# Optimization experiments

Hardware: AMD Instinct MI355X
Metric: run time of the kernel (lower is better)

The kernel has to match this reference:

```python
import jax, jax.numpy as jnp
import numpy as np

B, SQ, SKV, D = 4, 4096, 4096, 64

def setup_inputs() -> dict:
    key = jax.random.key(0)
    kq, kv = jax.random.split(key)
    query = jax.random.normal(kq, (B, SQ, D), dtype=jnp.float32)
    value = jax.random.normal(kv, (B, SKV, D), dtype=jnp.float32)
    return {"query": query, "value": value}

def reference(query, value):
    # scores = Q @ V^T  (value acts as both keys and values; no 1/sqrt(d) scaling)
    scores = jnp.einsum('bqd,bkd->bqk', query, value)  # [B, SQ, SKV]
    dist = jax.nn.softmax(scores, axis=-1)
    context = jnp.einsum('bqk,bkd->bqd', dist, value)  # [B, SQ, D]
    return context
```

## Files before the change

### kernel.cpp

```cpp
#include <hip/hip_runtime.h>


#define NB   4
#define SQ   4096
#define SKV  4096
#define DH   64
#define L2E  1.44269504088896340736f

typedef _Float16 half8 __attribute__((ext_vector_type(8)));
typedef _Float16 half4 __attribute__((ext_vector_type(4)));
typedef _Float16 half2v __attribute__((ext_vector_type(2)));
typedef float f32x4 __attribute__((ext_vector_type(4)));
typedef unsigned short u16;

#define MFMA16(a, b, c) __builtin_amdgcn_mfma_f32_16x16x16f16((a), (b), (c), 0, 0, 0)
#define MFMA32(a, b, c) __builtin_amdgcn_mfma_f32_16x16x32_f16((a), (b), (c), 0, 0, 0)

__device__ __forceinline__ u16 f2h(float f) {
  _Float16 h = (_Float16)f;
  return __builtin_bit_cast(u16, h);
}
__device__ __forceinline__ half2v pkrtz(float a, float b) {
  return __builtin_bit_cast(half2v, __builtin_amdgcn_cvt_pkrtz(a, b));
}

__global__ __launch_bounds__(256) void prep_kernel(
    const float* __restrict__ V, u16* __restrict__ vh, u16* __restrict__ vt) {
  __shared__ u16 ldsT[16 * 72];
  int blk = blockIdx.x;
  int b   = blk >> 8;
  int rem = blk & 255;
  int j0  = (rem >> 2) << 6;
  int d0  = (rem & 3) << 4;
  int t   = threadIdx.x;
  int j   = t >> 2;
  int dc  = (t & 3) << 2;

  const float* src = V + ((size_t)(b * SKV) + j0 + j) * DH + d0 + dc;
  float4 v4 = *(const float4*)src;
  u16 h[4] = {f2h(v4.x), f2h(v4.y), f2h(v4.z), f2h(v4.w)};
  unsigned p0 = (unsigned)h[0] | ((unsigned)h[1] << 16);
  unsigned p1 = (unsigned)h[2] | ((unsigned)h[3] << 16);
  size_t go = ((size_t)(b * SKV) + j0 + j) * DH + d0 + dc;
  *(uint2*)(vh + go) = make_uint2(p0, p1);

#pragma unroll
  for (int k = 0; k < 4; ++k) ldsT[(dc + k) * 72 + j] = h[k];
  __syncthreads();

  int dl = t >> 4;
  int jc = (t & 15) << 2;
  u16 tr[4];
#pragma unroll
  for (int k = 0; k < 4; ++k) tr[k] = ldsT[dl * 72 + jc + k];
  unsigned q0 = (unsigned)tr[0] | ((unsigned)tr[1] << 16);
  unsigned q1 = (unsigned)tr[2] | ((unsigned)tr[3] << 16);
  *(uint2*)(vt + ((size_t)(b * DH) + d0 + dl) * SKV + j0 + jc) = make_uint2(q0, q1);
}

__global__ __launch_bounds__(256, 4) void attn_kernel(
    const float* __restrict__ Q,
    const u16* __restrict__ vh,
    const u16* __restrict__ vt,
    u16* __restrict__ po,
    float* __restrict__ pm,
    float* __restrict__ pl,
    int S, int kvLen) {
  __shared__ __align__(16) u16 lds[2][2][64 * 72];

  int blk  = blockIdx.x;
  int tile = blk / S;
  int s    = blk - tile * S;
  int b    = tile >> 5;
  int q0   = (tile & 31) << 7;
  int kv0  = s * kvLen;
  int t    = threadIdx.x;
  int wave = t >> 6;
  int lane = t & 63;
  int col  = lane & 15;
  int quad = lane >> 4;
  int qw   = q0 + (wave << 5);

  half8 qf[2][2];
#pragma unroll
  for (int set = 0; set < 2; ++set) {
#pragma unroll
    for (int kc = 0; kc < 2; ++kc) {
      const float* qp = Q + ((size_t)(b * SQ) + qw + set * 16 + col) * DH +
                        kc * 32 + (quad << 3);
      float4 a0 = *(const float4*)qp;
      float4 a1 = *(const float4*)(qp + 4);
      half8 h;
      h[0] = (_Float16)(a0.x * L2E); h[1] = (_Float16)(a0.y * L2E);
      h[2] = (_Float16)(a0.z * L2E); h[3] = (_Float16)(a0.w * L2E);
      h[4] = (_Float16)(a1.x * L2E); h[5] = (_Float16)(a1.y * L2E);
      h[6] = (_Float16)(a1.z * L2E); h[7] = (_Float16)(a1.w * L2E);
      qf[set][kc] = h;
    }
  }

  f32x4 o[2][4];
  float m_r[2] = {-1e30f, -1e30f};
  float l_r[2] = {0.f, 0.f};
#pragma unroll
  for (int set = 0; set < 2; ++set)
#pragma unroll
    for (int nf = 0; nf < 4; ++nf) o[set][nf] = (f32x4){0.f, 0.f, 0.f, 0.f};

  int sr = t >> 2;
  int sc = (t & 3) << 4;
  const u16* gv  = vh + (size_t)(b * SKV) * DH;
  const u16* gvt = vt + (size_t)(b * DH) * SKV;
  int l0 = sr * 72 + sc;

  {
    size_t g  = (size_t)(kv0 + sr) * DH + sc;
    size_t gt = (size_t)sr * SKV + kv0 + sc;
    *(uint4*)(&lds[0][0][l0])     = *(const uint4*)(gv + g);
    *(uint4*)(&lds[0][0][l0 + 8]) = *(const uint4*)(gv + g + 8);
    *(uint4*)(&lds[0][1][l0])     = *(const uint4*)(gvt + gt);
    *(uint4*)(&lds[0][1][l0 + 8]) = *(const uint4*)(gvt + gt + 8);
  }

  int nIter = kvLen >> 6;
  int cur = 0;
  for (int it = 0; it < nIter; ++it) {
    __syncthreads();

    uint4 a0, a1, c0, c1;
    bool more = (it + 1) < nIter;
    if (more) {
      int j0n = kv0 + ((it + 1) << 6);
      size_t g  = (size_t)(j0n + sr) * DH + sc;
      size_t gt = (size_t)sr * SKV + j0n + sc;
      a0 = *(const uint4*)(gv + g);
      a1 = *(const uint4*)(gv + g + 8);
      c0 = *(const uint4*)(gvt + gt);
      c1 = *(const uint4*)(gvt + gt + 8);
    }

    const u16* sv  = &lds[cur][0][0];
    const u16* svt = &lds[cur][1][0];

    half4 pf[2][4];
#pragma unroll
    for (int set = 0; set < 2; ++set) {
      f32x4 sf[4];
#pragma unroll
      for (int nf = 0; nf < 4; ++nf) sf[nf] = (f32x4){0.f, 0.f, 0.f, 0.f};
#pragma unroll
      for (int nf = 0; nf < 4; ++nf) {
#pragma unroll
        for (int kc = 0; kc < 2; ++kc) {
          half8 av = *(const half8*)(sv + (nf * 16 + col) * 72 + kc * 32 + (quad << 3));
          sf[nf] = MFMA32(av, qf[set][kc], sf[nf]);
        }
      }

      float tm = sf[0][0];
#pragma unroll
      for (int nf = 0; nf < 4; ++nf)
#pragma unroll
        for (int r = 0; r < 4; ++r) tm = fmaxf(tm, sf[nf][r]);
      tm = fmaxf(tm, __shfl_xor(tm, 16, 64));
      tm = fmaxf(tm, __shfl_xor(tm, 32, 64));
      float mn = fmaxf(m_r[set], tm);
      float al = exp2f(m_r[set] - mn);
      m_r[set] = mn;
      float rs = 0.f;
#pragma unroll
      for (int nf = 0; nf < 4; ++nf) {
        float p0 = exp2f(sf[nf][0] - mn);
        float p1 = exp2f(sf[nf][1] - mn);
        float p2 = exp2f(sf[nf][2] - mn);
        float p3 = exp2f(sf[nf][3] - mn);
        rs += (p0 + p1) + (p2 + p3);
        half2v lo = pkrtz(p0, p1);
        half2v hi = pkrtz(p2, p3);
        pf[set][nf] = __builtin_shufflevector(lo, hi, 0, 1, 2, 3);
      }
      l_r[set] = l_r[set] * al + rs;
#pragma unroll
      for (int nf = 0; nf < 4; ++nf)
#pragma unroll
        for (int r = 0; r < 4; ++r) o[set][nf][r] *= al;
    }

#pragma unroll
    for (int kc4 = 0; kc4 < 4; ++kc4) {
#pragma unroll
      for (int nf2 = 0; nf2 < 4; ++nf2) {
        half4 avt = *(const half4*)(svt + (nf2 * 16 + col) * 72 + kc4 * 16 + (quad << 2));
        o[0][nf2] = MFMA16(avt, pf[0][kc4], o[0][nf2]);
        o[1][nf2] = MFMA16(avt, pf[1][kc4], o[1][nf2]);
      }
    }

    if (more) {
      u16* dv  = &lds[cur ^ 1][0][0];
      u16* dvt = &lds[cur ^ 1][1][0];
      *(uint4*)(dv + l0)      = a0;
      *(uint4*)(dv + l0 + 8)  = a1;
      *(uint4*)(dvt + l0)     = c0;
      *(uint4*)(dvt + l0 + 8) = c1;
    }
    cur ^= 1;
  }

#pragma unroll
  for (int set = 0; set < 2; ++set) {
    l_r[set] += __shfl_xor(l_r[set], 16, 64);
    l_r[set] += __shfl_xor(l_r[set], 32, 64);
  }
  int pidx = tile * S + s;
  if (quad == 0) {
#pragma unroll
    for (int set = 0; set < 2; ++set) {
      int row = (wave << 5) + set * 16 + col;
      pm[(size_t)pidx * 128 + row] = m_r[set];
      pl[(size_t)pidx * 128 + row] = l_r[set];
    }
  }

  __syncthreads();
  u16* tp = &lds[0][0][0];
#pragma unroll
  for (int set = 0; set < 2; ++set) {
    int q = (wave << 5) + set * 16 + col;
#pragma unroll
    for (int nf2 = 0; nf2 < 4; ++nf2) {
#pragma unroll
      for (int r2 = 0; r2 < 4; r2 += 2) {
        unsigned pk = (unsigned)f2h(o[set][nf2][r2]) |
                      ((unsigned)f2h(o[set][nf2][r2 + 1]) << 16);
        int d = nf2 * 16 + (quad << 2) + r2;
        *(unsigned*)(tp + q * 72 + d) = pk;
      }
    }
  }
  __syncthreads();
  {
    u16* pob = po + (size_t)pidx * 128 * 64;
    int q = t >> 1, hc = (t & 1) << 5;
    uint4 x0 = *(const uint4*)(tp + q * 72 + hc);
    uint4 x1 = *(const uint4*)(tp + q * 72 + hc + 8);
    uint4 x2 = *(const uint4*)(tp + q * 72 + hc + 16);
    uint4 x3 = *(const uint4*)(tp + q * 72 + hc + 24);
    *(uint4*)(pob + q * 64 + hc)      = x0;
    *(uint4*)(pob + q * 64 + hc + 8)  = x1;
    *(uint4*)(pob + q * 64 + hc + 16) = x2;
    *(uint4*)(pob + q * 64 + hc + 24) = x3;
  }
}

__global__ __launch_bounds__(256) void combine_kernel(
    const u16* __restrict__ po,
    const float* __restrict__ pm,
    const float* __restrict__ pl,
    float* __restrict__ out, int S) {
  int t    = threadIdx.x;
  int rowg = blockIdx.x * 32 + (t >> 3);
  int tile = rowg >> 7;
  int row  = rowg & 127;
  int dc   = (t & 7) << 3;

  float mv[8], lv[8];
  float M = -1e30f;
  for (int s = 0; s < S; ++s) {
    mv[s] = pm[(size_t)(tile * S + s) * 128 + row];
    lv[s] = pl[(size_t)(tile * S + s) * 128 + row];
    M = fmaxf(M, mv[s]);
  }
  float L = 0.f, w[8];
  for (int s = 0; s < S; ++s) {
    w[s] = exp2f(mv[s] - M);
    L += lv[s] * w[s];
  }
  float acc[8] = {0.f, 0.f, 0.f, 0.f, 0.f, 0.f, 0.f, 0.f};
  for (int s = 0; s < S; ++s) {
    const u16* p = po + (size_t)(tile * S + s) * 8192 + row * 64 + dc;
    uint4 raw = *(const uint4*)p;
    half8 x = __builtin_bit_cast(half8, raw);
#pragma unroll
    for (int k = 0; k < 8; ++k) acc[k] += w[s] * (float)x[k];
  }
  float invL = 1.0f / L;
  float* op = out + (size_t)rowg * 64 + dc;
  f32x4 o0 = (f32x4){acc[0], acc[1], acc[2], acc[3]};
  f32x4 o1 = (f32x4){acc[4], acc[5], acc[6], acc[7]};
  *(f32x4*)op       = o0 * invL;
  *(f32x4*)(op + 4) = o1 * invL;
}

extern "C" void kernel_launch(void* const* d_in, const int* in_sizes, int n_in,
                              void* d_out, int out_size, void* d_ws, size_t ws_size,
                              hipStream_t stream) {
  const float* Q = (const float*)d_in[0];
  const float* V = (const float*)d_in[1];
  float* out = (float*)d_out;

  const size_t convBytes = (size_t)2 * NB * SKV * DH * 2;
  auto partBytes = [](int S) {
    return (size_t)NB * 32 * S * ((size_t)128 * 64 * 2 + 128 * 8);
  };
  int S = 8;
  while (S > 1 && ws_size < convBytes + partBytes(S)) S >>= 1;
  int kvLen = SKV / S;

  u16* vh = (u16*)d_ws;
  u16* vt = vh + (size_t)NB * SKV * DH;
  u16* po = vt + (size_t)NB * SKV * DH;
  float* pm = (float*)(po + (size_t)NB * 32 * S * 128 * 64);
  float* pl = pm + (size_t)NB * 32 * S * 128;

  prep_kernel<<<NB * 256, 256, 0, stream>>>(V, vh, vt);
  attn_kernel<<<NB * 32 * S, 256, 0, stream>>>(Q, vh, vt, po, pm, pl, S, kvLen);
  combine_kernel<<<NB * SQ / 32, 256, 0, stream>>>(po, pm, pl, out, S);
}
```

Baseline: 128.3 us.

## Load K/V tiles via global_load_lds DMA with XOR-swizzled layout and smaller query tiles

The prep kernel now writes V and V^T with an XOR-swizzled 8-element chunk order, so the attention kernel can copy tiles straight into unpadded LDS using global_load_lds (bypassing registers) and still read them without bank conflicts. The attention block shrinks from 128 to 64 query rows, one 16-row set per wave, and the KV split factor drops from 8 to 4. Per-wave register use goes down, and the global-to-LDS copies no longer go through VGPRs or need explicit LDS stores. In exchange, each block has less reuse of every loaded KV tile, so the same total KV traffic through LDS is spread over twice as many query tiles. Correctness depends on the DMA lane-to-LDS address mapping matching the swizzle.

```diff
diff --git a/kernel.cpp b/kernel.cpp
--- a/kernel.cpp
+++ b/kernel.cpp
@@ -22,6 +22,12 @@
 }
 __device__ __forceinline__ half2v pkrtz(float a, float b) {
   return __builtin_bit_cast(half2v, __builtin_amdgcn_cvt_pkrtz(a, b));
+}
+
+typedef __attribute__((address_space(1))) void gvoid;
+typedef __attribute__((address_space(3))) void lvoid;
+__device__ __forceinline__ void dma16(const u16* g, u16* l) {
+  __builtin_amdgcn_global_load_lds((gvoid*)g, (lvoid*)l, 16, 0, 0);
 }
 
 __global__ __launch_bounds__(256) void prep_kernel(
@@ -41,8 +47,9 @@
   u16 h[4] = {f2h(v4.x), f2h(v4.y), f2h(v4.z), f2h(v4.w)};
   unsigned p0 = (unsigned)h[0] | ((unsigned)h[1] << 16);
   unsigned p1 = (unsigned)h[2] | ((unsigned)h[3] << 16);
-  size_t go = ((size_t)(b * SKV) + j0 + j) * DH + d0 + dc;
-  *(uint2*)(vh + go) = make_uint2(p0, p1);
+  int dfull = d0 + dc;
+  int physd = ((((dfull >> 3) ^ (j & 7)) << 3)) + (dfull & 7);
+  *(uint2*)(vh + ((size_t)(b * SKV) + j0 + j) * DH + physd) = make_uint2(p0, p1);
 
 #pragma unroll
   for (int k = 0; k < 4; ++k) ldsT[(dc + k) * 72 + j] = h[k];
@@ -55,7 +62,13 @@
   for (int k = 0; k < 4; ++k) tr[k] = ldsT[dl * 72 + jc + k];
   unsigned q0 = (unsigned)tr[0] | ((unsigned)tr[1] << 16);
   unsigned q1 = (unsigned)tr[2] | ((unsigned)tr[3] << 16);
-  *(uint2*)(vt + ((size_t)(b * DH) + d0 + dl) * SKV + j0 + jc) = make_uint2(q0, q1);
+  int d   = d0 + dl;
+  int kc2 = jc >> 5;
+  int g   = (jc >> 4) & 1;
+  int qd  = (jc >> 2) & 3;
+  int hp  = ((kc2 << 2) | qd) ^ (d & 7);
+  *(uint2*)(vt + ((size_t)(b * DH) + d) * SKV + j0 + (hp << 3) + (g << 2)) =
+      make_uint2(q0, q1);
 }
 
 __global__ __launch_bounds__(256, 4) void attn_kernel(
@@ -66,97 +79,86 @@
     float* __restrict__ pm,
     float* __restrict__ pl,
     int S, int kvLen) {
-  __shared__ __align__(16) u16 lds[2][2][64 * 72];
+  __shared__ __align__(16) u16 lds[2][2][4096];
 
   int blk  = blockIdx.x;
   int tile = blk / S;
   int s    = blk - tile * S;
-  int b    = tile >> 5;
-  int q0   = (tile & 31) << 7;
+  int b    = tile >> 6;
+  int q0   = (tile & 63) << 6;
   int kv0  = s * kvLen;
   int t    = threadIdx.x;
   int wave = t >> 6;
   int lane = t & 63;
   int col  = lane & 15;
   int quad = lane >> 4;
-  int qw   = q0 + (wave << 5);
-
-  half8 qf[2][2];
-#pragma unroll
-  for (int set = 0; set < 2; ++set) {
-#pragma unroll
-    for (int kc = 0; kc < 2; ++kc) {
-      const float* qp = Q + ((size_t)(b * SQ) + qw + set * 16 + col) * DH +
-                        kc * 32 + (quad << 3);
-      float4 a0 = *(const float4*)qp;
-      float4 a1 = *(const float4*)(qp + 4);
-      half8 h;
-      h[0] = (_Float16)(a0.x * L2E); h[1] = (_Float16)(a0.y * L2E);
-      h[2] = (_Float16)(a0.z * L2E); h[3] = (_Float16)(a0.w * L2E);
-      h[4] = (_Float16)(a1.x * L2E); h[5] = (_Float16)(a1.y * L2E);
-      h[6] = (_Float16)(a1.z * L2E); h[7] = (_Float16)(a1.w * L2E);
-      qf[set][kc] = h;
-    }
-  }
-
-  f32x4 o[2][4];
-  float m_r[2] = {-1e30f, -1e30f};
-  float l_r[2] = {0.f, 0.f};
-#pragma unroll
-  for (int set = 0; set < 2; ++set)
-#pragma unroll
-    for (int nf = 0; nf < 4; ++nf) o[set][nf] = (f32x4){0.f, 0.f, 0.f, 0.f};
-
-  int sr = t >> 2;
-  int sc = (t & 3) << 4;
+  int qw   = q0 + (wave << 4);
+  int c7   = col & 7;
+
   const u16* gv  = vh + (size_t)(b * SKV) * DH;
   const u16* gvt = vt + (size_t)(b * DH) * SKV;
-  int l0 = sr * 72 + sc;
-
-  {
-    size_t g  = (size_t)(kv0 + sr) * DH + sc;
-    size_t gt = (size_t)sr * SKV + kv0 + sc;
-    *(uint4*)(&lds[0][0][l0])     = *(const uint4*)(gv + g);
-    *(uint4*)(&lds[0][0][l0 + 8]) = *(const uint4*)(gv + g + 8);
-    *(uint4*)(&lds[0][1][l0])     = *(const uint4*)(gvt + gt);
-    *(uint4*)(&lds[0][1][l0 + 8]) = *(const uint4*)(gvt + gt + 8);
-  }
+
+  int r0 = t >> 3;
+  int c0 = (t & 7) << 3;
+  int wb = wave << 9;
+
+  half8 qf[2];
+#pragma unroll
+  for (int kc = 0; kc < 2; ++kc) {
+    const float* qp = Q + ((size_t)(b * SQ) + qw + col) * DH + kc * 32 + (quad << 3);
+    float4 a0 = *(const float4*)qp;
+    float4 a1 = *(const float4*)(qp + 4);
+    half8 hq;
+    hq[0] = (_Float16)(a0.x * L2E); hq[1] = (_Float16)(a0.y * L2E);
+    hq[2] = (_Float16)(a0.z * L2E); hq[3] = (_Float16)(a0.w * L2E);
+    hq[4] = (_Float16)(a1.x * L2E); hq[5] = (_Float16)(a1.y * L2E);
+    hq[6] = (_Float16)(a1.z * L2E); hq[7] = (_Float16)(a1.w * L2E);
+    qf[kc] = hq;
+  }
+
+  f32x4 o[4];
+#pragma unroll
+  for (int nf = 0; nf < 4; ++nf) o[nf] = (f32x4){0.f, 0.f, 0.f, 0.f};
+  float m_r = -1e30f, l_r = 0.f;
+
+  dma16(gv + ((size_t)(kv0 + r0) << 6) + c0,       &lds[0][0][0] + wb);
+  dma16(gv + ((size_t)(kv0 + r0 + 32) << 6) + c0,  &lds[0][0][0] + 2048 + wb);
+  dma16(gvt + (size_t)r0 * SKV + kv0 + c0,         &lds[0][1][0] + wb);
+  dma16(gvt + (size_t)(r0 + 32) * SKV + kv0 + c0,  &lds[0][1][0] + 2048 + wb);
 
   int nIter = kvLen >> 6;
   int cur = 0;
   for (int it = 0; it < nIter; ++it) {
     __syncthreads();
 
-    uint4 a0, a1, c0, c1;
-    bool more = (it + 1) < nIter;
-    if (more) {
+    if ((it + 1) < nIter) {
       int j0n = kv0 + ((it + 1) << 6);
-      size_t g  = (size_t)(j0n + sr) * DH + sc;
-      size_t gt = (size_t)sr * SKV + j0n + sc;
-      a0 = *(const uint4*)(gv + g);
-      a1 = *(const uint4*)(gv + g + 8);
-      c0 = *(const uint4*)(gvt + gt);
-      c1 = *(const uint4*)(gvt + gt + 8);
-    }
-
-    const u16* sv  = &lds[cur][0][0];
-    const u16* svt = &lds[cur][1][0];
-
-    half4 pf[2][4];
-#pragma unroll
-    for (int set = 0; set < 2; ++set) {
-      f32x4 sf[4];
-#pragma unroll
-      for (int nf = 0; nf < 4; ++nf) sf[nf] = (f32x4){0.f, 0.f, 0.f, 0.f};
-#pragma unroll
-      for (int nf = 0; nf < 4; ++nf) {
-#pragma unroll
-        for (int kc = 0; kc < 2; ++kc) {
-          half8 av = *(const half8*)(sv + (nf * 16 + col) * 72 + kc * 32 + (quad << 3));
-          sf[nf] = MFMA32(av, qf[set][kc], sf[nf]);
-        }
+      u16* dv  = &lds[cur ^ 1][0][0];
+      u16* dvt = &lds[cur ^ 1][1][0];
+      dma16(gv + ((size_t)(j0n + r0) << 6) + c0,      dv + wb);
+      dma16(gv + ((size_t)(j0n + r0 + 32) << 6) + c0, dv + 2048 + wb);
+      dma16(gvt + (size_t)r0 * SKV + j0n + c0,        dvt + wb);
+      dma16(gvt + (size_t)(r0 + 32) * SKV + j0n + c0, dvt + 2048 + wb);
+    }
+
+    const u16* sv = &lds[cur][0][0];
+    const u16* st = &lds[cur][1][0];
+
+    f32x4 sf[4];
+#pragma unroll
+    for (int nf = 0; nf < 4; ++nf) sf[nf] = (f32x4){0.f, 0.f, 0.f, 0.f};
+#pragma unroll
+    for (int nf = 0; nf < 4; ++nf) {
+#pragma unroll
+      for (int kc = 0; kc < 2; ++kc) {
+        int ch = ((kc << 2) | quad) ^ c7;
+        half8 av = *(const half8*)(sv + ((nf * 16 + col) << 6) + (ch << 3));
+        sf[nf] = MFMA32(av, qf[kc], sf[nf]);
       }
-
+    }
+
+    half4 pf[4];
+    {
       float tm = sf[0][0];
 #pragma unroll
       for (int nf = 0; nf < 4; ++nf)
@@ -164,9 +166,9 @@
         for (int r = 0; r < 4; ++r) tm = fmaxf(tm, sf[nf][r]);
       tm = fmaxf(tm, __shfl_xor(tm, 16, 64));
       tm = fmaxf(tm, __shfl_xor(tm, 32, 64));
-      float mn = fmaxf(m_r[set], tm);
-      float al = exp2f(m_r[set] - mn);
-      m_r[set] = mn;
+      float mn = fmaxf(m_r, tm);
+      float al = exp2f(m_r - mn);
+      m_r = mn;
       float rs = 0.f;
 #pragma unroll
       for (int nf = 0; nf < 4; ++nf) {
@@ -177,79 +179,62 @@
         rs += (p0 + p1) + (p2 + p3);
         half2v lo = pkrtz(p0, p1);
         half2v hi = pkrtz(p2, p3);
-        pf[set][nf] = __builtin_shufflevector(lo, hi, 0, 1, 2, 3);
+        pf[nf] = __builtin_shufflevector(lo, hi, 0, 1, 2, 3);
       }
-      l_r[set] = l_r[set] * al + rs;
+      l_r = l_r * al + rs;
 #pragma unroll
       for (int nf = 0; nf < 4; ++nf)
 #pragma unroll
-        for (int r = 0; r < 4; ++r) o[set][nf][r] *= al;
-    }
-
-#pragma unroll
-    for (int kc4 = 0; kc4 < 4; ++kc4) {
+        for (int r = 0; r < 4; ++r) o[nf][r] *= al;
+    }
+
+#pragma unroll
+    for (int kc2 = 0; kc2 < 2; ++kc2) {
 #pragma unroll
       for (int nf2 = 0; nf2 < 4; ++nf2) {
-        half4 avt = *(const half4*)(svt + (nf2 * 16 + col) * 72 + kc4 * 16 + (quad << 2));
-        o[0][nf2] = MFMA16(avt, pf[0][kc4], o[0][nf2]);
-        o[1][nf2] = MFMA16(avt, pf[1][kc4], o[1][nf2]);
+        int ch = ((kc2 << 2) | quad) ^ c7;
+        half8 w8 = *(const half8*)(st + ((nf2 * 16 + col) << 6) + (ch << 3));
+        half4 wlo = __builtin_shufflevector(w8, w8, 0, 1, 2, 3);
+        half4 whi = __builtin_shufflevector(w8, w8, 4, 5, 6, 7);
+        o[nf2] = MFMA16(wlo, pf[kc2 * 2], o[nf2]);
+        o[nf2] = MFMA16(whi, pf[kc2 * 2 + 1], o[nf2]);
       }
     }
 
-    if (more) {
-      u16* dv  = &lds[cur ^ 1][0][0];
-      u16* dvt = &lds[cur ^ 1][1][0];
-      *(uint4*)(dv + l0)      = a0;
-      *(uint4*)(dv + l0 + 8)  = a1;
-      *(uint4*)(dvt + l0)     = c0;
-      *(uint4*)(dvt + l0 + 8) = c1;
-    }
     cur ^= 1;
   }
 
-#pragma unroll
-  for (int set = 0; set < 2; ++set) {
-    l_r[set] += __shfl_xor(l_r[set], 16, 64);
-    l_r[set] += __shfl_xor(l_r[set], 32, 64);
-  }
+  l_r += __shfl_xor(l_r, 16, 64);
+  l_r += __shfl_xor(l_r, 32, 64);
   int pidx = tile * S + s;
   if (quad == 0) {
-#pragma unroll
-    for (int set = 0; set < 2; ++set) {
-      int row = (wave << 5) + set * 16 + col;
-      pm[(size_t)pidx * 128 + row] = m_r[set];
-      pl[(size_t)pidx * 128 + row] = l_r[set];
-    }
+    pm[(size_t)pidx * 64 + (wave << 4) + col] = m_r;
+    pl[(size_t)pidx * 64 + (wave << 4) + col] = l_r;
   }
 
   __syncthreads();
   u16* tp = &lds[0][0][0];
-#pragma unroll
-  for (int set = 0; set < 2; ++set) {
-    int q = (wave << 5) + set * 16 + col;
+  {
+    int qrow = (wave << 4) + col;
 #pragma unroll
     for (int nf2 = 0; nf2 < 4; ++nf2) {
 #pragma unroll
       for (int r2 = 0; r2 < 4; r2 += 2) {
-        unsigned pk = (unsigned)f2h(o[set][nf2][r2]) |
-                      ((unsigned)f2h(o[set][nf2][r2 + 1]) << 16);
+        unsigned pk = (unsigned)f2h(o[nf2][r2]) |
+                      ((unsigned)f2h(o[nf2][r2 + 1]) << 16);
         int d = nf2 * 16 + (quad << 2) + r2;
-        *(unsigned*)(tp + q * 72 + d) = pk;
+        *(unsigned*)(tp + qrow * 72 + d) = pk;
       }
     }
   }
   __syncthreads();
   {
-    u16* pob = po + (size_t)pidx * 128 * 64;
-    int q = t >> 1, hc = (t & 1) << 5;
+    u16* pob = po + (size_t)pidx * 64 * 64;
+    int q = t >> 2, hc = (t & 3) << 4;
     uint4 x0 = *(const uint4*)(tp + q * 72 + hc);
     uint4 x1 = *(const uint4*)(tp + q * 72 + hc + 8);
-    uint4 x2 = *(const uint4*)(tp + q * 72 + hc + 16);
-    uint4 x3 = *(const uint4*)(tp + q * 72 + hc + 24);
-    *(uint4*)(pob + q * 64 + hc)      = x0;
-    *(uint4*)(pob + q * 64 + hc + 8)  = x1;
-    *(uint4*)(pob + q * 64 + hc + 16) = x2;
-    *(uint4*)(pob + q * 64 + hc + 24) = x3;
+    *(uint4*)(pob + q * 64 + hc)     = x0;
+    *(uint4*)(pob + q * 64 + hc + 8) = x1;
   }
 }
 
@@ -260,15 +245,15 @@
     float* __restrict__ out, int S) {
   int t    = threadIdx.x;
   int rowg = blockIdx.x * 32 + (t >> 3);
-  int tile = rowg >> 7;
-  int row  = rowg & 127;
+  int tile = rowg >> 6;
+  int row  = rowg & 63;
   int dc   = (t & 7) << 3;
 
   float mv[8], lv[8];
   float M = -1e30f;
   for (int s = 0; s < S; ++s) {
-    mv[s] = pm[(size_t)(tile * S + s) * 128 + row];
-    lv[s] = pl[(size_t)(tile * S + s) * 128 + row];
+    mv[s] = pm[(size_t)(tile * S + s) * 64 + row];
+    lv[s] = pl[(size_t)(tile * S + s) * 64 + row];
     M = fmaxf(M, mv[s]);
   }
   float L = 0.f, w[8];
@@ -278,7 +263,7 @@
   }
   float acc[8] = {0.f, 0.f, 0.f, 0.f, 0.f, 0.f, 0.f, 0.f};
   for (int s = 0; s < S; ++s) {
-    const u16* p = po + (size_t)(tile * S + s) * 8192 + row * 64 + dc;
+    const u16* p = po + (size_t)(tile * S + s) * 4096 + row * 64 + dc;
     uint4 raw = *(const uint4*)p;
     half8 x = __builtin_bit_cast(half8, raw);
 #pragma unroll
@@ -301,19 +286,19 @@
 
   const size_t convBytes = (size_t)2 * NB * SKV * DH * 2;
   auto partBytes = [](int S) {
-    return (size_t)NB * 32 * S * ((size_t)128 * 64 * 2 + 128 * 8);
+    return (size_t)NB * 64 * S * ((size_t)64 * 64 * 2 + 64 * 8);
   };
-  int S = 8;
+  int S = 4;
   while (S > 1 && ws_size < convBytes + partBytes(S)) S >>= 1;
   int kvLen = SKV / S;
 
   u16* vh = (u16*)d_ws;
   u16* vt = vh + (size_t)NB * SKV * DH;
   u16* po = vt + (size_t)NB * SKV * DH;
-  float* pm = (float*)(po + (size_t)NB * 32 * S * 128 * 64);
-  float* pl = pm + (size_t)NB * 32 * S * 128;
+  float* pm = (float*)(po + (size_t)NB * 64 * S * 64 * 64);
+  float* pl = pm + (size_t)NB * 64 * S * 64;
 
   prep_kernel<<<NB * 256, 256, 0, stream>>>(V, vh, vt);
-  attn_kernel<<<NB * 32 * S, 256, 0, stream>>>(Q, vh, vt, po, pm, pl, S, kvLen);
+  attn_kernel<<<NB * 64 * S, 256, 0, stream>>>(Q, vh, vt, po, pm, pl, S, kvLen);
   combine_kernel<<<NB * SQ / 32, 256, 0, stream>>>(po, pm, pl, out, S);
 }
```

After: 106.0 us. 1.21x faster.
